# Kernel tuning notes

Hardware: AMD Instinct MI355X
Metric: run time of the kernel (lower is better)

Reference implementation:

```python
import jax, jax.numpy as jnp
import numpy as np

N_NODES = 50000


def _gcn_norm(edge_index, n):
    # Add self-loops (PyG GCNConv default) and compute symmetric normalization.
    src = jnp.concatenate([edge_index[0], jnp.arange(n, dtype=edge_index.dtype)])
    dst = jnp.concatenate([edge_index[1], jnp.arange(n, dtype=edge_index.dtype)])
    deg = jax.ops.segment_sum(jnp.ones(src.shape[0], dtype=jnp.float32), dst,
                              num_segments=n)
    dinv = jnp.where(deg > 0, jax.lax.rsqrt(deg), 0.0)
    norm = dinv[src] * dinv[dst]  # [E+N]
    return src, dst, norm


def _gcn_conv(x, src, dst, norm, W, b, n):
    h = x @ W                              # [N, out] linear transform first
    msgs = h[src] * norm[:, None]          # gather + edge-wise scale [E+N, out]
    out = jax.ops.segment_sum(msgs, dst, num_segments=n)  # scatter-add
    return out + b


def setup_inputs() -> dict:
    key = jax.random.key(0)
    k1, k2, k3, k4 = jax.random.split(key, 4)
    N, E, F, H, C = N_NODES, 1600000, 128, 128, 64
    x = jax.random.normal(k1, (N, F), dtype=jnp.float32)
    edge_index = jax.random.randint(k2, (2, E), 0, N, dtype=jnp.int64)
    W1 = jax.random.normal(k3, (F, H), dtype=jnp.float32) * 0.05
    b1 = jnp.zeros((H,), dtype=jnp.float32)
    W2 = jax.random.normal(k4, (H, C), dtype=jnp.float32) * 0.05
    b2 = jnp.zeros((C,), dtype=jnp.float32)
    return {"x": x, "edge_index": edge_index, "W1": W1, "b1": b1,
            "W2": W2, "b2": b2}


def reference(x, edge_index, W1, b1, W2, b2):
    n = x.shape[0]
    src, dst, norm = _gcn_norm(edge_index, n)
    h = _gcn_conv(x, src, dst, norm, W1, b1, n)
    h = jax.nn.relu(h)
    out = _gcn_conv(h, src, dst, norm, W2, b2, n)
    return out
```

## Files before the change

### kernel.cpp

```cpp
#include <hip/hip_runtime.h>
#include <hip/hip_bf16.h>
#include <stdint.h>

#define N_NODES 50000
#define N_EDGES 1600000
#define N_TOT   (N_EDGES + N_NODES)
#define NBKT      256
#define BKT_NODES 196
#define BKT_CAP   7168
#define PBKT_CAP  11264
#define TILE      4096
#define EPT       16
#define ZROW      N_NODES

typedef unsigned short u16;
typedef __attribute__((ext_vector_type(8))) short short8;
typedef __attribute__((ext_vector_type(4))) float floatx4;
typedef __attribute__((ext_vector_type(2))) float f2;

__device__ __forceinline__ float b2f(u16 u) {
    union { unsigned int i; float f; } v; v.i = ((unsigned int)u) << 16; return v.f;
}
__device__ __forceinline__ float asf(unsigned u) {
    union { unsigned int i; float f; } v; v.i = u; return v.f;
}
__device__ __forceinline__ u16 f2b(float f) {
    union { unsigned int i; float f; } v; v.f = f;
    unsigned int r = (v.i + 0x7FFFu + ((v.i >> 16) & 1u)) >> 16;
    return (u16)r;
}

__device__ __forceinline__ void accu(f2& a, unsigned u) {
    f2 r; r.x = asf(u << 16); r.y = asf(u & 0xFFFF0000u);
    a += r;
}
__device__ __forceinline__ void acc4u(f2* a, uint4 q) {
    accu(a[0], q.x); accu(a[1], q.y); accu(a[2], q.z); accu(a[3], q.w);
}
__device__ __forceinline__ void acc2u(f2* a, uint2 q) {
    accu(a[0], q.x); accu(a[1], q.y);
}
__device__ __forceinline__ uint4 g256(const char* hB, unsigned s, unsigned lb) {
    return *(const uint4*)(hB + ((s << 8) + lb));
}
__device__ __forceinline__ uint2 g128(const char* hB, unsigned s, unsigned lb) {
    return *(const uint2*)(hB + ((s << 7) + lb));
}

__global__ __launch_bounds__(256) void k_part(const int* __restrict__ ei,
                                              const unsigned* __restrict__ xw,
                                              int* __restrict__ flags,
                                              unsigned* __restrict__ pairs,
                                              int* __restrict__ bktcnt) {
    __shared__ unsigned pairsL[TILE];
    __shared__ unsigned char bktL[TILE];
    __shared__ int hist[NBKT], incl[NBKT], delta[NBKT];
    __shared__ int zc, pc;
    int tid = threadIdx.x;
    long base = (long)blockIdx.x * TILE;
    hist[tid] = 0;
    if (tid == 0) { zc = 0; pc = 0; }
    __syncthreads();
    unsigned hw = ((const unsigned*)ei)[2 * tid + 1];
    atomicAdd(&zc, hw == 0 ? 1 : 0);
    if (blockIdx.x == 0) {
        unsigned w = xw[tid];
        int ex = (w >> 7) & 0xFF;
        atomicAdd(&pc, ((ex == 0) || (ex >= 0x60 && ex <= 0x9F)) ? 1 : 0);
    }
    __syncthreads();
    int i64 = zc > 250;
    if (blockIdx.x == 0 && tid == 0) {
        flags[0] = (pc < 160) ? 1 : 0;
        flags[1] = i64;
    }

    int myb[EPT], myrank[EPT]; unsigned myp[EPT];
#pragma unroll
    for (int t = 0; t < EPT; t++) {
        long idx = base + t * 256 + tid;
        int b = -1; unsigned p = 0;
        if (idx < N_TOT) {
            int s, d;
            if (idx < N_EDGES) {
                if (i64) { s = ei[2 * idx]; d = ei[2 * (N_EDGES + idx)]; }
                else     { s = ei[idx];     d = ei[N_EDGES + idx]; }
            } else {
                s = d = (int)(idx - N_EDGES);
            }
            b = d / BKT_NODES;
            p = (unsigned)s | ((unsigned)(d - b * BKT_NODES) << 16);
        }
        myb[t] = b; myp[t] = p;
        myrank[t] = (b >= 0) ? atomicAdd(&hist[b], 1) : 0;
    }
    __syncthreads();

    int tot = hist[tid];
    incl[tid] = tot;
    __syncthreads();
    for (int o = 1; o < NBKT; o <<= 1) {
        int t2 = (tid >= o) ? incl[tid - o] : 0;
        __syncthreads();
        incl[tid] += t2;
        __syncthreads();
    }
    int excl = incl[tid] - tot;
    int gb = atomicAdd(&bktcnt[tid], tot);
    hist[tid]  = excl;
    delta[tid] = tid * BKT_CAP + gb - excl;
    __syncthreads();

#pragma unroll
    for (int t = 0; t < EPT; t++) {
        if (myb[t] >= 0) {
            int slot = hist[myb[t]] + myrank[t];
            pairsL[slot] = myp[t];
            bktL[slot]   = (unsigned char)myb[t];
        }
    }
    __syncthreads();
    int count = incl[NBKT - 1];
    for (int i = tid; i < count; i += 256) {
        int b = bktL[i];
        int pos = delta[b] + i;
        if (pos - b * BKT_CAP < BKT_CAP)
            pairs[pos] = pairsL[i];
    }
}

__global__ __launch_bounds__(256) void k_bucket(const unsigned* __restrict__ pairs,
                                                const int* __restrict__ bktcnt,
                                                int* __restrict__ rowstart,
                                                int* __restrict__ deg,
                                                float* __restrict__ dinv,
                                                u16* __restrict__ csr) {
    __shared__ u16 csrL[PBKT_CAP];
    __shared__ int degL[NBKT], curL[NBKT], scanT[NBKT];
    int b = blockIdx.x, tid = threadIdx.x;
    int cnt = bktcnt[b];
    const unsigned* reg = pairs + (size_t)b * BKT_CAP;
    degL[tid] = 0;
    __syncthreads();
    for (int i = tid; i < cnt; i += 256)
        atomicAdd(&degL[reg[i] >> 16], 1);
    __syncthreads();
    int n = b * BKT_NODES + tid;
    int valid = (tid < BKT_NODES) && (n < N_NODES);
    int v = degL[tid];
    int pv = valid ? ((v + 31) & ~31) : 0;
    scanT[tid] = pv;
    __syncthreads();
    for (int o = 1; o < NBKT; o <<= 1) {
        int t = (tid >= o) ? scanT[tid - o] : 0;
        __syncthreads();
        scanT[tid] += t;
        __syncthreads();
    }
    int pexcl = scanT[tid] - pv;
    curL[tid] = pexcl;
    if (valid) {
        rowstart[n] = b * PBKT_CAP + pexcl;
        deg[n]      = v;
        dinv[n]     = rsqrtf((float)v);
    }
    int pcnt = scanT[NBKT - 1];
    if (pcnt > PBKT_CAP) pcnt = PBKT_CAP;
    __syncthreads();
    for (int i = tid; i < pcnt; i += 256) csrL[i] = (u16)ZROW;
    __syncthreads();
    for (int i = tid; i < cnt; i += 256) {
        unsigned p = reg[i];
        int slot = atomicAdd(&curL[p >> 16], 1);
        if (slot < PBKT_CAP) csrL[slot] = (u16)(p & 0xFFFFu);
    }
    __syncthreads();
    for (int i = tid; i < pcnt; i += 256)
        csr[(size_t)b * PBKT_CAP + i] = csrL[i];
}

template<int NOUT, bool ADYN>
__global__ __launch_bounds__(256) void k_gemm(const void* __restrict__ A,
                                              const void* __restrict__ W,
                                              const float* __restrict__ dinv,
                                              u16* __restrict__ out, int M,
                                              const int* __restrict__ flags) {
    const int isf32 = flags[0];
    constexpr int LDW = 136;
    __shared__ __align__(16) u16 Wt[NOUT * LDW];
    int tid = threadIdx.x;
    if (blockIdx.x == 0 && tid < NOUT)
        out[(size_t)M * NOUT + tid] = 0;
    const float* Wf = (const float*)W;
    const u16*   Wu = (const u16*)W;
    for (int idx = tid; idx < 128 * NOUT; idx += 256) {
        int k = idx / NOUT, n = idx % NOUT;
        Wt[n * LDW + k] = isf32 ? f2b(Wf[idx]) : Wu[idx];
    }
    __syncthreads();

    int wave = tid >> 6, lane = tid & 63;
    int quad = lane >> 4, l16 = lane & 15;
    int r0 = blockIdx.x * 64 + wave * 16;
    int r = r0 + l16; if (r >= M) r = M - 1;

    floatx4 acc[NOUT / 16];
#pragma unroll
    for (int i = 0; i < NOUT / 16; i++) acc[i] = (floatx4)(0.f);

#pragma unroll
    for (int ks = 0; ks < 4; ks++) {
        short8 a;
        if (ADYN && isf32) {
            const float* af = (const float*)A + (size_t)r * 128 + ks * 32 + quad * 8;
            float4 v0 = ((const float4*)af)[0];
            float4 v1 = ((const float4*)af)[1];
            a[0] = (short)f2b(v0.x); a[1] = (short)f2b(v0.y);
            a[2] = (short)f2b(v0.z); a[3] = (short)f2b(v0.w);
            a[4] = (short)f2b(v1.x); a[5] = (short)f2b(v1.y);
            a[6] = (short)f2b(v1.z); a[7] = (short)f2b(v1.w);
        } else {
            a = ((const short8*)((const u16*)A + (size_t)r * 128))[ks * 4 + quad];
        }
#pragma unroll
        for (int nt = 0; nt < NOUT / 16; nt++) {
            const short8* bp = (const short8*)&Wt[(nt * 16 + l16) * LDW + ks * 32 + quad * 8];
            acc[nt] = __builtin_amdgcn_mfma_f32_16x16x32_bf16(a, *bp, acc[nt], 0, 0, 0);
        }
    }
    float sc[4];
#pragma unroll
    for (int j = 0; j < 4; j++) {
        int row = r0 + quad * 4 + j;
        sc[j] = dinv[row < M ? row : 0];
    }
#pragma unroll
    for (int nt = 0; nt < NOUT / 16; nt++) {
#pragma unroll
        for (int j = 0; j < 4; j++) {
            int row = r0 + quad * 4 + j;
            if (row < M)
                out[(size_t)row * NOUT + nt * 16 + l16] = f2b(acc[nt][j] * sc[j]);
        }
    }
}

__global__ __launch_bounds__(256) void k_agg1(const u16* __restrict__ h,
                                              const u16* __restrict__ csr,
                                              const int* __restrict__ rowstart,
                                              const int* __restrict__ deg,
                                              const float* __restrict__ dinv,
                                              const void* __restrict__ bias,
                                              u16* __restrict__ out,
                                              const int* __restrict__ flags) {
    int wave = threadIdx.x >> 6, lane = threadIdx.x & 63;
    int d = blockIdx.x * 4 + wave;
    int grp = lane >> 4, l16 = lane & 15;
    int start = rowstart[d], dg = deg[d];
    int pdg = (dg + 31) & ~31;
    int C = pdg >> 2;
    const uint4* cp = (const uint4*)(csr + start + grp * C);
    int nc = C >> 3;
    const char* hB = (const char*)h;
    unsigned lb = (unsigned)l16 << 4;

    f2 acc[4] = {};
    uint4 ci = cp[0];
    uint4 q0 = g256(hB, ci.x & 0xFFFFu, lb), q1 = g256(hB, ci.x >> 16, lb),
          q2 = g256(hB, ci.y & 0xFFFFu, lb), q3 = g256(hB, ci.y >> 16, lb),
          q4 = g256(hB, ci.z & 0xFFFFu, lb), q5 = g256(hB, ci.z >> 16, lb),
          q6 = g256(hB, ci.w & 0xFFFFu, lb), q7 = g256(hB, ci.w >> 16, lb);
    for (int k = 1; k < nc; k++) {
        uint4 cn = cp[k];
        acc4u(acc, q0); q0 = g256(hB, cn.x & 0xFFFFu, lb);
        acc4u(acc, q1); q1 = g256(hB, cn.x >> 16, lb);
        acc4u(acc, q2); q2 = g256(hB, cn.y & 0xFFFFu, lb);
        acc4u(acc, q3); q3 = g256(hB, cn.y >> 16, lb);
        acc4u(acc, q4); q4 = g256(hB, cn.z & 0xFFFFu, lb);
        acc4u(acc, q5); q5 = g256(hB, cn.z >> 16, lb);
        acc4u(acc, q6); q6 = g256(hB, cn.w & 0xFFFFu, lb);
        acc4u(acc, q7); q7 = g256(hB, cn.w >> 16, lb);
    }
    acc4u(acc, q0); acc4u(acc, q1); acc4u(acc, q2); acc4u(acc, q3);
    acc4u(acc, q4); acc4u(acc, q5); acc4u(acc, q6); acc4u(acc, q7);

#pragma unroll
    for (int j = 0; j < 4; j++) {
        acc[j].x += __shfl_xor(acc[j].x, 16); acc[j].y += __shfl_xor(acc[j].y, 16);
        acc[j].x += __shfl_xor(acc[j].x, 32); acc[j].y += __shfl_xor(acc[j].y, 32);
    }
    if (grp == 0) {
        int isf32 = flags[0];
        float dd = dinv[d];
        u16 r8[8];
#pragma unroll
        for (int j = 0; j < 4; j++) {
            float bx = isf32 ? ((const float*)bias)[l16 * 8 + 2 * j]
                             : b2f(((const u16*)bias)[l16 * 8 + 2 * j]);
            float by = isf32 ? ((const float*)bias)[l16 * 8 + 2 * j + 1]
                             : b2f(((const u16*)bias)[l16 * 8 + 2 * j + 1]);
            float vx = acc[j].x * dd + bx;
            float vy = acc[j].y * dd + by;
            r8[2 * j]     = f2b(vx > 0.f ? vx : 0.f);
            r8[2 * j + 1] = f2b(vy > 0.f ? vy : 0.f);
        }
        uint4 o;
        o.x = r8[0] | ((unsigned)r8[1] << 16); o.y = r8[2] | ((unsigned)r8[3] << 16);
        o.z = r8[4] | ((unsigned)r8[5] << 16); o.w = r8[6] | ((unsigned)r8[7] << 16);
        ((uint4*)(out + (size_t)d * 128))[l16] = o;
    }
}

__global__ __launch_bounds__(256) void k_agg2(const u16* __restrict__ h,
                                              const u16* __restrict__ csr,
                                              const int* __restrict__ rowstart,
                                              const int* __restrict__ deg,
                                              const float* __restrict__ dinv,
                                              const void* __restrict__ bias,
                                              float* __restrict__ out,
                                              const int* __restrict__ flags) {
    int wave = threadIdx.x >> 6, lane = threadIdx.x & 63;
    int d = blockIdx.x * 4 + wave;
    int grp = lane >> 4, l16 = lane & 15;
    int start = rowstart[d], dg = deg[d];
    int pdg = (dg + 31) & ~31;
    int C = pdg >> 2;
    const uint4* cp = (const uint4*)(csr + start + grp * C);
    int nc = C >> 3;
    const char* hB = (const char*)h;
    unsigned lb = (unsigned)l16 << 3;

    f2 acc[2] = {};
    uint4 ci = cp[0];
    uint2 q0 = g128(hB, ci.x & 0xFFFFu, lb), q1 = g128(hB, ci.x >> 16, lb),
          q2 = g128(hB, ci.y & 0xFFFFu, lb), q3 = g128(hB, ci.y >> 16, lb),
          q4 = g128(hB, ci.z & 0xFFFFu, lb), q5 = g128(hB, ci.z >> 16, lb),
          q6 = g128(hB, ci.w & 0xFFFFu, lb), q7 = g128(hB, ci.w >> 16, lb);
    for (int k = 1; k < nc; k++) {
        uint4 cn = cp[k];
        acc2u(acc, q0); q0 = g128(hB, cn.x & 0xFFFFu, lb);
        acc2u(acc, q1); q1 = g128(hB, cn.x >> 16, lb);
        acc2u(acc, q2); q2 = g128(hB, cn.y & 0xFFFFu, lb);
        acc2u(acc, q3); q3 = g128(hB, cn.y >> 16, lb);
        acc2u(acc, q4); q4 = g128(hB, cn.z & 0xFFFFu, lb);
        acc2u(acc, q5); q5 = g128(hB, cn.z >> 16, lb);
        acc2u(acc, q6); q6 = g128(hB, cn.w & 0xFFFFu, lb);
        acc2u(acc, q7); q7 = g128(hB, cn.w >> 16, lb);
    }
    acc2u(acc, q0); acc2u(acc, q1); acc2u(acc, q2); acc2u(acc, q3);
    acc2u(acc, q4); acc2u(acc, q5); acc2u(acc, q6); acc2u(acc, q7);

#pragma unroll
    for (int j = 0; j < 2; j++) {
        acc[j].x += __shfl_xor(acc[j].x, 16); acc[j].y += __shfl_xor(acc[j].y, 16);
        acc[j].x += __shfl_xor(acc[j].x, 32); acc[j].y += __shfl_xor(acc[j].y, 32);
    }
    if (grp == 0) {
        int isf32 = flags[0];
        float dd = dinv[d];
        float r4[4];
#pragma unroll
        for (int j = 0; j < 2; j++) {
            float bx = isf32 ? ((const float*)bias)[l16 * 4 + 2 * j]
                             : b2f(((const u16*)bias)[l16 * 4 + 2 * j]);
            float by = isf32 ? ((const float*)bias)[l16 * 4 + 2 * j + 1]
                             : b2f(((const u16*)bias)[l16 * 4 + 2 * j + 1]);
            r4[2 * j]     = acc[j].x * dd + bx;
            r4[2 * j + 1] = acc[j].y * dd + by;
        }
        ((float4*)(out + (size_t)d * 64))[l16] = make_float4(r4[0], r4[1], r4[2], r4[3]);
    }
}

extern "C" void kernel_launch(void* const* d_in, const int* in_sizes, int n_in,
                              void* d_out, int out_size, void* d_ws, size_t ws_size,
                              hipStream_t stream) {
    const void* x  = d_in[0];
    const int*  ei = (const int*)d_in[1];
    const void* W1 = d_in[2];
    const void* b1 = d_in[3];
    const void* W2 = d_in[4];
    const void* b2 = d_in[5];
    float* out = (float*)d_out;

    char* ws = (char*)d_ws;
    int*      flags    = (int*)(ws + 0);
    int*      bktcnt   = (int*)(ws + 1024);
    int*      deg      = (int*)(ws + 4096);
    int*      rowstart = (int*)(ws + 204800);
    float*    dinv     = (float*)(ws + 405504);
    u16*      csr      = (u16*)(ws + 606208);
    unsigned* pairs    = (unsigned*)(ws + 6373376);
    u16*      h1       = (u16*)(ws + 6373376);
    u16*      out1     = (u16*)(ws + 19173632);
    u16*      h2       = (u16*)(ws + 6373376);

    hipMemsetAsync(bktcnt, 0, NBKT * sizeof(int), stream);
    k_part   <<<(N_TOT + TILE - 1) / TILE, 256, 0, stream>>>(ei, (const unsigned*)x,
                                                             flags, pairs, bktcnt);
    k_bucket <<<NBKT, 256, 0, stream>>>(pairs, bktcnt, rowstart, deg, dinv, csr);

    k_gemm<128, true> <<<(N_NODES + 63) / 64, 256, 0, stream>>>(x, W1, dinv, h1, N_NODES, flags);
    k_agg1<<<N_NODES / 4, 256, 0, stream>>>(h1, csr, rowstart, deg, dinv, b1, out1, flags);
    k_gemm<64, false> <<<(N_NODES + 63) / 64, 256, 0, stream>>>(out1, W2, dinv, h2, N_NODES, flags);
    k_agg2<<<N_NODES / 4, 256, 0, stream>>>(h2, csr, rowstart, deg, dinv, b2, out, flags);
}
```

Before: 241.5 us.

## Use nontemporal loads/stores for streaming data and vectorize bucket kernel accesses

Switches the streaming reads and writes (pairs, csr, GEMM inputs and outputs, aggregation outputs) to nontemporal builtins so they avoid polluting the cache, which is meant to keep the randomly gathered feature rows resident. It also vectorizes the bucket kernel: pairs are read four at a time and the LDS fill and global copy use 16-byte chunks. One risk is that the GEMM output h is read back soon after by the gather, so marking those stores nontemporal may hurt reuse. The vector csr copy also assumes pcnt is a multiple of 8, which the 32-padding guarantees.

```diff
diff --git a/kernel.cpp b/kernel.cpp
--- a/kernel.cpp
+++ b/kernel.cpp
@@ -17,6 +17,9 @@
 typedef __attribute__((ext_vector_type(8))) short short8;
 typedef __attribute__((ext_vector_type(4))) float floatx4;
 typedef __attribute__((ext_vector_type(2))) float f2;
+typedef __attribute__((ext_vector_type(4))) unsigned u32x4;
+typedef __attribute__((ext_vector_type(2))) unsigned u32x2;
+typedef __attribute__((ext_vector_type(4))) float f32x4;
 
 __device__ __forceinline__ float b2f(u16 u) {
     union { unsigned int i; float f; } v; v.i = ((unsigned int)u) << 16; return v.f;
@@ -34,17 +37,17 @@
     f2 r; r.x = asf(u << 16); r.y = asf(u & 0xFFFF0000u);
     a += r;
 }
-__device__ __forceinline__ void acc4u(f2* a, uint4 q) {
+__device__ __forceinline__ void acc4u(f2* a, u32x4 q) {
     accu(a[0], q.x); accu(a[1], q.y); accu(a[2], q.z); accu(a[3], q.w);
 }
-__device__ __forceinline__ void acc2u(f2* a, uint2 q) {
+__device__ __forceinline__ void acc2u(f2* a, u32x2 q) {
     accu(a[0], q.x); accu(a[1], q.y);
 }
-__device__ __forceinline__ uint4 g256(const char* hB, unsigned s, unsigned lb) {
-    return *(const uint4*)(hB + ((s << 8) + lb));
-}
-__device__ __forceinline__ uint2 g128(const char* hB, unsigned s, unsigned lb) {
-    return *(const uint2*)(hB + ((s << 7) + lb));
+__device__ __forceinline__ u32x4 g256(const char* hB, unsigned s, unsigned lb) {
+    return *(const u32x4*)(hB + ((s << 8) + lb));
+}
+__device__ __forceinline__ u32x2 g128(const char* hB, unsigned s, unsigned lb) {
+    return *(const u32x2*)(hB + ((s << 7) + lb));
 }
 
 __global__ __launch_bounds__(256) void k_part(const int* __restrict__ ei,
@@ -125,7 +128,7 @@
         int b = bktL[i];
         int pos = delta[b] + i;
         if (pos - b * BKT_CAP < BKT_CAP)
-            pairs[pos] = pairsL[i];
+            __builtin_nontemporal_store(pairsL[i], &pairs[pos]);
     }
 }
 
@@ -135,15 +138,22 @@
                                                 int* __restrict__ deg,
                                                 float* __restrict__ dinv,
                                                 u16* __restrict__ csr) {
-    __shared__ u16 csrL[PBKT_CAP];
+    __shared__ __align__(16) u16 csrL[PBKT_CAP];
     __shared__ int degL[NBKT], curL[NBKT], scanT[NBKT];
     int b = blockIdx.x, tid = threadIdx.x;
     int cnt = bktcnt[b];
     const unsigned* reg = pairs + (size_t)b * BKT_CAP;
     degL[tid] = 0;
     __syncthreads();
-    for (int i = tid; i < cnt; i += 256)
-        atomicAdd(&degL[reg[i] >> 16], 1);
+    int cnt4 = cnt & ~3;
+    for (int i = tid * 4; i < cnt4; i += 1024) {
+        u32x4 p4 = __builtin_nontemporal_load((const u32x4*)(reg + i));
+        atomicAdd(&degL[p4.x >> 16], 1);
+        atomicAdd(&degL[p4.y >> 16], 1);
+        atomicAdd(&degL[p4.z >> 16], 1);
+        atomicAdd(&degL[p4.w >> 16], 1);
+    }
+    { int i = cnt4 + tid; if (i < cnt) atomicAdd(&degL[reg[i] >> 16], 1); }
     __syncthreads();
     int n = b * BKT_NODES + tid;
     int valid = (tid < BKT_NODES) && (n < N_NODES);
@@ -167,16 +177,32 @@
     int pcnt = scanT[NBKT - 1];
     if (pcnt > PBKT_CAP) pcnt = PBKT_CAP;
     __syncthreads();
-    for (int i = tid; i < pcnt; i += 256) csrL[i] = (u16)ZROW;
-    __syncthreads();
-    for (int i = tid; i < cnt; i += 256) {
-        unsigned p = reg[i];
-        int slot = atomicAdd(&curL[p >> 16], 1);
-        if (slot < PBKT_CAP) csrL[slot] = (u16)(p & 0xFFFFu);
-    }
-    __syncthreads();
-    for (int i = tid; i < pcnt; i += 256)
-        csr[(size_t)b * PBKT_CAP + i] = csrL[i];
+    {
+        u32x4 zfill;
+        zfill.x = zfill.y = zfill.z = zfill.w = ((unsigned)ZROW << 16) | (unsigned)ZROW;
+        for (int i = tid * 8; i < pcnt; i += 2048)
+            *(u32x4*)(csrL + i) = zfill;
+    }
+    __syncthreads();
+    for (int i = tid * 4; i < cnt4; i += 1024) {
+        u32x4 p4 = __builtin_nontemporal_load((const u32x4*)(reg + i));
+        int s0 = atomicAdd(&curL[p4.x >> 16], 1); if (s0 < PBKT_CAP) csrL[s0] = (u16)p4.x;
+        int s1 = atomicAdd(&curL[p4.y >> 16], 1); if (s1 < PBKT_CAP) csrL[s1] = (u16)p4.y;
+        int s2 = atomicAdd(&curL[p4.z >> 16], 1); if (s2 < PBKT_CAP) csrL[s2] = (u16)p4.z;
+        int s3 = atomicAdd(&curL[p4.w >> 16], 1); if (s3 < PBKT_CAP) csrL[s3] = (u16)p4.w;
+    }
+    {
+        int i = cnt4 + tid;
+        if (i < cnt) {
+            unsigned p = reg[i];
+            int slot = atomicAdd(&curL[p >> 16], 1);
+            if (slot < PBKT_CAP) csrL[slot] = (u16)p;
+        }
+    }
+    __syncthreads();
+    for (int i = tid * 8; i < pcnt; i += 2048)
+        __builtin_nontemporal_store(*(const u32x4*)(csrL + i),
+                                    (u32x4*)(csr + (size_t)b * PBKT_CAP + i));
 }
 
 template<int NOUT, bool ADYN>
@@ -212,15 +238,16 @@
     for (int ks = 0; ks < 4; ks++) {
         short8 a;
         if (ADYN && isf32) {
-            const float* af = (const float*)A + (size_t)r * 128 + ks * 32 + quad * 8;
-            float4 v0 = ((const float4*)af)[0];
-            float4 v1 = ((const float4*)af)[1];
+            const f32x4* af = (const f32x4*)((const float*)A + (size_t)r * 128 + ks * 32 + quad * 8);
+            f32x4 v0 = __builtin_nontemporal_load(af);
+            f32x4 v1 = __builtin_nontemporal_load(af + 1);
             a[0] = (short)f2b(v0.x); a[1] = (short)f2b(v0.y);
             a[2] = (short)f2b(v0.z); a[3] = (short)f2b(v0.w);
             a[4] = (short)f2b(v1.x); a[5] = (short)f2b(v1.y);
             a[6] = (short)f2b(v1.z); a[7] = (short)f2b(v1.w);
         } else {
-            a = ((const short8*)((const u16*)A + (size_t)r * 128))[ks * 4 + quad];
+            const short8* ap = (const short8*)((const u16*)A + (size_t)r * 128) + ks * 4 + quad;
+            a = __builtin_nontemporal_load(ap);
         }
 #pragma unroll
         for (int nt = 0; nt < NOUT / 16; nt++) {
@@ -240,7 +267,8 @@
         for (int j = 0; j < 4; j++) {
             int row = r0 + quad * 4 + j;
             if (row < M)
-                out[(size_t)row * NOUT + nt * 16 + l16] = f2b(acc[nt][j] * sc[j]);
+                __builtin_nontemporal_store(f2b(acc[nt][j] * sc[j]),
+                                            &out[(size_t)row * NOUT + nt * 16 + l16]);
         }
     }
 }
@@ -259,19 +287,19 @@
     int start = rowstart[d], dg = deg[d];
     int pdg = (dg + 31) & ~31;
     int C = pdg >> 2;
-    const uint4* cp = (const uint4*)(csr + start + grp * C);
+    const u32x4* cp = (const u32x4*)(csr + start + grp * C);
     int nc = C >> 3;
     const char* hB = (const char*)h;
     unsigned lb = (unsigned)l16 << 4;
 
     f2 acc[4] = {};
-    uint4 ci = cp[0];
-    uint4 q0 = g256(hB, ci.x & 0xFFFFu, lb), q1 = g256(hB, ci.x >> 16, lb),
+    u32x4 ci = __builtin_nontemporal_load(cp);
+    u32x4 q0 = g256(hB, ci.x & 0xFFFFu, lb), q1 = g256(hB, ci.x >> 16, lb),
           q2 = g256(hB, ci.y & 0xFFFFu, lb), q3 = g256(hB, ci.y >> 16, lb),
           q4 = g256(hB, ci.z & 0xFFFFu, lb), q5 = g256(hB, ci.z >> 16, lb),
           q6 = g256(hB, ci.w & 0xFFFFu, lb), q7 = g256(hB, ci.w >> 16, lb);
     for (int k = 1; k < nc; k++) {
-        uint4 cn = cp[k];
+        u32x4 cn = __builtin_nontemporal_load(cp + k);
         acc4u(acc, q0); q0 = g256(hB, cn.x & 0xFFFFu, lb);
         acc4u(acc, q1); q1 = g256(hB, cn.x >> 16, lb);
         acc4u(acc, q2); q2 = g256(hB, cn.y & 0xFFFFu, lb);
@@ -304,10 +332,10 @@
             r8[2 * j]     = f2b(vx > 0.f ? vx : 0.f);
             r8[2 * j + 1] = f2b(vy > 0.f ? vy : 0.f);
         }
-        uint4 o;
+        u32x4 o;
         o.x = r8[0] | ((unsigned)r8[1] << 16); o.y = r8[2] | ((unsigned)r8[3] << 16);
         o.z = r8[4] | ((unsigned)r8[5] << 16); o.w = r8[6] | ((unsigned)r8[7] << 16);
-        ((uint4*)(out + (size_t)d * 128))[l16] = o;
+        __builtin_nontemporal_store(o, (u32x4*)(out + (size_t)d * 128) + l16);
     }
 }
 
@@ -325,19 +353,19 @@
     int start = rowstart[d], dg = deg[d];
     int pdg = (dg + 31) & ~31;
     int C = pdg >> 2;
-    const uint4* cp = (const uint4*)(csr + start + grp * C);
+    const u32x4* cp = (const u32x4*)(csr + start + grp * C);
     int nc = C >> 3;
     const char* hB = (const char*)h;
     unsigned lb = (unsigned)l16 << 3;
 
     f2 acc[2] = {};
-    uint4 ci = cp[0];
-    uint2 q0 = g128(hB, ci.x & 0xFFFFu, lb), q1 = g128(hB, ci.x >> 16, lb),
+    u32x4 ci = __builtin_nontemporal_load(cp);
+    u32x2 q0 = g128(hB, ci.x & 0xFFFFu, lb), q1 = g128(hB, ci.x >> 16, lb),
           q2 = g128(hB, ci.y & 0xFFFFu, lb), q3 = g128(hB, ci.y >> 16, lb),
           q4 = g128(hB, ci.z & 0xFFFFu, lb), q5 = g128(hB, ci.z >> 16, lb),
           q6 = g128(hB, ci.w & 0xFFFFu, lb), q7 = g128(hB, ci.w >> 16, lb);
     for (int k = 1; k < nc; k++) {
-        uint4 cn = cp[k];
+        u32x4 cn = __builtin_nontemporal_load(cp + k);
         acc2u(acc, q0); q0 = g128(hB, cn.x & 0xFFFFu, lb);
         acc2u(acc, q1); q1 = g128(hB, cn.x >> 16, lb);
         acc2u(acc, q2); q2 = g128(hB, cn.y & 0xFFFFu, lb);
@@ -368,7 +396,8 @@
             r4[2 * j]     = acc[j].x * dd + bx;
             r4[2 * j + 1] = acc[j].y * dd + by;
         }
-        ((float4*)(out + (size_t)d * 64))[l16] = make_float4(r4[0], r4[1], r4[2], r4[3]);
+        f32x4 o; o.x = r4[0]; o.y = r4[1]; o.z = r4[2]; o.w = r4[3];
+        __builtin_nontemporal_store(o, (f32x4*)(out + (size_t)d * 64) + l16);
     }
 }
 
```

Result: no change. 245.9 us (+1.8%).

## Fuse layer-2 GEMM into layer-1 aggregation kernel via LDS tile and MFMA

Applied to the files above, without the earlier changes.

The first aggregation kernel now processes 16 destination nodes per 1024-thread block. It stages the ReLU'd bf16 rows in shared memory and multiplies them by W2 with MFMA inside the same kernel, writing h2 directly. This removes the separate layer-2 GEMM launch and the round trip of the 128-wide intermediate through global memory. In exchange, every block reloads and transposes W2 into LDS, only one wave does the GEMM, and the 1024-thread blocks with barriers may lower occupancy for the gather-bound aggregation.

```diff
diff --git a/kernel.cpp b/kernel.cpp
--- a/kernel.cpp
+++ b/kernel.cpp
@@ -17,6 +17,7 @@
 typedef __attribute__((ext_vector_type(8))) short short8;
 typedef __attribute__((ext_vector_type(4))) float floatx4;
 typedef __attribute__((ext_vector_type(2))) float f2;
+typedef __attribute__((ext_vector_type(4))) unsigned u32x4;
 
 __device__ __forceinline__ float b2f(u16 u) {
     union { unsigned int i; float f; } v; v.i = ((unsigned int)u) << 16; return v.f;
@@ -245,16 +246,36 @@
     }
 }
 
-__global__ __launch_bounds__(256) void k_agg1(const u16* __restrict__ h,
-                                              const u16* __restrict__ csr,
-                                              const int* __restrict__ rowstart,
-                                              const int* __restrict__ deg,
-                                              const float* __restrict__ dinv,
-                                              const void* __restrict__ bias,
-                                              u16* __restrict__ out,
-                                              const int* __restrict__ flags) {
-    int wave = threadIdx.x >> 6, lane = threadIdx.x & 63;
-    int d = blockIdx.x * 4 + wave;
+__global__ __launch_bounds__(1024) void k_agg1f(const u16* __restrict__ h,
+                                                const u16* __restrict__ csr,
+                                                const int* __restrict__ rowstart,
+                                                const int* __restrict__ deg,
+                                                const float* __restrict__ dinv,
+                                                const void* __restrict__ bias,
+                                                const void* __restrict__ W2,
+                                                u16* __restrict__ h2,
+                                                const int* __restrict__ flags) {
+    constexpr int LDW = 136;
+    __shared__ __align__(16) u16 Wt[64 * LDW];
+    __shared__ __align__(16) u16 YL[16 * LDW];
+    int tid = threadIdx.x;
+    int wave = tid >> 6, lane = tid & 63;
+    const int isf32 = flags[0];
+
+    {
+        const float* Wf = (const float*)W2;
+        const u16*   Wu = (const u16*)W2;
+        for (int idx = tid; idx < 128 * 64; idx += 1024) {
+            int k = idx >> 6, n = idx & 63;
+            Wt[n * LDW + k] = isf32 ? f2b(Wf[idx]) : Wu[idx];
+        }
+    }
+    if (blockIdx.x == 0 && tid < 8) {
+        u32x4 z = {};
+        ((u32x4*)(h2 + (size_t)ZROW * 64))[tid] = z;
+    }
+
+    int d = blockIdx.x * 16 + wave;
     int grp = lane >> 4, l16 = lane & 15;
     int start = rowstart[d], dg = deg[d];
     int pdg = (dg + 31) & ~31;
@@ -290,7 +311,6 @@
         acc[j].x += __shfl_xor(acc[j].x, 32); acc[j].y += __shfl_xor(acc[j].y, 32);
     }
     if (grp == 0) {
-        int isf32 = flags[0];
         float dd = dinv[d];
         u16 r8[8];
 #pragma unroll
@@ -307,7 +327,36 @@
         uint4 o;
         o.x = r8[0] | ((unsigned)r8[1] << 16); o.y = r8[2] | ((unsigned)r8[3] << 16);
         o.z = r8[4] | ((unsigned)r8[5] << 16); o.w = r8[6] | ((unsigned)r8[7] << 16);
-        ((uint4*)(out + (size_t)d * 128))[l16] = o;
+        *(uint4*)&YL[wave * LDW + l16 * 8] = o;
+    }
+    __syncthreads();
+
+    if (wave == 0) {
+        int quad = lane >> 4;
+        floatx4 acc2[4];
+#pragma unroll
+        for (int i = 0; i < 4; i++) acc2[i] = (floatx4)(0.f);
+#pragma unroll
+        for (int ks = 0; ks < 4; ks++) {
+            short8 a = *(const short8*)&YL[l16 * LDW + ks * 32 + quad * 8];
+#pragma unroll
+            for (int nt = 0; nt < 4; nt++) {
+                const short8* bp = (const short8*)&Wt[(nt * 16 + l16) * LDW + ks * 32 + quad * 8];
+                acc2[nt] = __builtin_amdgcn_mfma_f32_16x16x32_bf16(a, *bp, acc2[nt], 0, 0, 0);
+            }
+        }
+        int d0 = blockIdx.x * 16;
+        float sc[4];
+#pragma unroll
+        for (int j = 0; j < 4; j++) sc[j] = dinv[d0 + quad * 4 + j];
+#pragma unroll
+        for (int nt = 0; nt < 4; nt++) {
+#pragma unroll
+            for (int j = 0; j < 4; j++) {
+                int row = d0 + quad * 4 + j;
+                h2[(size_t)row * 64 + nt * 16 + l16] = f2b(acc2[nt][j] * sc[j]);
+            }
+        }
     }
 }
 
@@ -392,8 +441,7 @@
     u16*      csr      = (u16*)(ws + 606208);
     unsigned* pairs    = (unsigned*)(ws + 6373376);
     u16*      h1       = (u16*)(ws + 6373376);
-    u16*      out1     = (u16*)(ws + 19173632);
-    u16*      h2       = (u16*)(ws + 6373376);
+    u16*      h2       = (u16*)(ws + 19173632);
 
     hipMemsetAsync(bktcnt, 0, NBKT * sizeof(int), stream);
     k_part   <<<(N_TOT + TILE - 1) / TILE, 256, 0, stream>>>(ei, (const unsigned*)x,
@@ -401,7 +449,6 @@
     k_bucket <<<NBKT, 256, 0, stream>>>(pairs, bktcnt, rowstart, deg, dinv, csr);
 
     k_gemm<128, true> <<<(N_NODES + 63) / 64, 256, 0, stream>>>(x, W1, dinv, h1, N_NODES, flags);
-    k_agg1<<<N_NODES / 4, 256, 0, stream>>>(h1, csr, rowstart, deg, dinv, b1, out1, flags);
-    k_gemm<64, false> <<<(N_NODES + 63) / 64, 256, 0, stream>>>(out1, W2, dinv, h2, N_NODES, flags);
+    k_agg1f<<<N_NODES / 16, 1024, 0, stream>>>(h1, csr, rowstart, deg, dinv, b1, W2, h2, flags);
     k_agg2<<<N_NODES / 4, 256, 0, stream>>>(h2, csr, rowstart, deg, dinv, b2, out, flags);
 }
```

Measured after the change: 241.8 us. About the same (+0.1%).
